# Kernel tuning notes

Hardware: AMD Instinct MI355X
Metric: run time of the kernel (lower is better)

## Reference

```python
import jax, jax.numpy as jnp
import numpy as np


def setup_inputs() -> dict:
    key = jax.random.key(0)
    ks = jax.random.split(key, 10)
    n_cells, n_genes, d, E = 10000, 2000, 128, 2000000
    return {
        "ufeats": jax.random.normal(ks[0], (n_cells, d), jnp.float32),
        "ifeats": jax.random.normal(ks[1], (n_genes, d), jnp.float32),
        "ge_factor": jax.random.uniform(ks[2], (n_genes, 1), jnp.float32),
        "sz_factor": jax.random.uniform(ks[3], (n_cells, 1), jnp.float32),
        "W_mean": jax.random.normal(ks[4], (d, 1), jnp.float32),
        "b_mean": jnp.zeros((1,), jnp.float32),
        "W_disp": jax.random.normal(ks[5], (d, 1), jnp.float32),
        "b_disp": jnp.zeros((1,), jnp.float32),
        "W_pi": jax.random.normal(ks[6], (d, 1), jnp.float32),
        "b_pi": jnp.zeros((1,), jnp.float32),
        "src_idx": jax.random.randint(ks[7], (E,), 0, n_cells, jnp.int64 if jax.config.read('jax_enable_x64') else jnp.int32),
        "dst_idx": jax.random.randint(ks[8], (E,), 0, n_genes, jnp.int64 if jax.config.read('jax_enable_x64') else jnp.int32),
    }


def reference(ufeats, ifeats, ge_factor, sz_factor,
              W_mean, b_mean, W_disp, b_disp, W_pi, b_pi,
              src_idx, dst_idx):
    # u_mul_v('h','h'): per-edge elementwise product of cell (u) and gene (v) feats -> [E, d]
    h_d = ufeats[src_idx] * ifeats[dst_idx]
    mu_ = jax.nn.sigmoid(h_d @ W_mean + b_mean)   # dec_mean: Linear + Sigmoid -> [E, 1]
    disp_ = h_d @ W_disp + b_disp                  # dec_disp: Linear -> [E, 1]
    pi = jax.nn.sigmoid(h_d @ W_pi + b_pi)         # dec_pi: Linear + Sigmoid -> [E, 1]
    gef = ge_factor[dst_idx]                       # u_mul_v('one','ge_factor') -> gene factor per edge
    szf = sz_factor[src_idx]                       # u_mul_v('sz_factor','one') -> cell size factor per edge
    disp = jnp.clip(jax.nn.softplus(gef * disp_), 1e-4, 1e4)          # DispAct
    mu = szf * jnp.clip(jnp.exp(gef * mu_) - 1.0, 1e-5, 1e6)          # MeanAct * sz_factor
    return (mu, disp, pi)
```

## Files before the change

kernel.cpp:

```cpp
#include <hip/hip_runtime.h>
#include <math.h>


typedef _Float16 f16x8 __attribute__((ext_vector_type(8)));
typedef float f32x4 __attribute__((ext_vector_type(4)));
typedef _Float16 h2 __attribute__((ext_vector_type(2)));
union U16 { uint4 u; f16x8 v; };
union HU { uint u; h2 h; };

__global__ __launch_bounds__(256) void cvt_f16_fused_kernel(
    const float4* __restrict__ srcA, int nA4,
    const float4* __restrict__ srcB, int nB4,
    uint2* __restrict__ dst)
{
    int i = blockIdx.x * blockDim.x + threadIdx.x;
    if (i >= nA4 + nB4) return;
    float4 f = (i < nA4) ? srcA[i] : srcB[i - nA4];
    HU a, b;
    a.h = h2{(_Float16)f.x, (_Float16)f.y};
    b.h = h2{(_Float16)f.z, (_Float16)f.w};
    dst[i] = make_uint2(a.u, b.u);
}

__global__ __launch_bounds__(256, 4) void zinb_mfma_lds_kernel(
    const _Float16* __restrict__ uhalf,
    const _Float16* __restrict__ ihalf,
    const float* __restrict__ ge_factor,
    const float* __restrict__ sz_factor,
    const float* __restrict__ W_mean, const float* __restrict__ b_mean,
    const float* __restrict__ W_disp, const float* __restrict__ b_disp,
    const float* __restrict__ W_pi,   const float* __restrict__ b_pi,
    const int* __restrict__ src_idx,
    const int* __restrict__ dst_idx,
    float* __restrict__ out,
    int E)
{
    const int tid  = threadIdx.x;
    const int lane = tid & 63;
    const int col  = lane & 15;
    const int kg   = lane >> 4;
    const int w    = (blockIdx.x * blockDim.x + tid) >> 6;
    const int nw   = (gridDim.x * blockDim.x) >> 6;
    const int ntiles = E >> 4;

    __shared__ __align__(16) _Float16 hsm[4][2048];
    char* const lds = (char*)hsm[tid >> 6];

    const char* const ubase = (const char*)uhalf;
    const char* const vbase = (const char*)ihalf;

    f16x8 bfrag[4];
    {
        const float* Wsel = (col == 0) ? W_mean : (col == 1) ? W_disp : W_pi;
#pragma unroll
        for (int c = 0; c < 4; ++c) {
            f16x8 b;
#pragma unroll
            for (int i = 0; i < 8; ++i) {
                const float wv = Wsel[32 * c + 8 * kg + i];
                b[i] = (col < 3) ? (_Float16)wv : (_Float16)0.f;
            }
            bfrag[c] = b;
        }
    }
    const float bm = b_mean[0], bd = b_disp[0], bp = b_pi[0];

    int wofs[4], rofs[4];
#pragma unroll
    for (int j = 0; j < 4; ++j) {
        const int row = kg + 4 * j;
        wofs[j] = row * 256 + ((col * 16) ^ ((row & 7) << 4));
    }
#pragma unroll
    for (int c = 0; c < 4; ++c)
        rofs[c] = col * 256 + (((c << 6) + (kg << 4)) ^ ((col & 7) << 4));

    int se_c = 0, de_c = 0, se_n = 0, de_n = 0;
    U16 uR[4], vR[4];
    if (w < ntiles) {
        se_c = src_idx[(w << 4) + col];
        de_c = dst_idx[(w << 4) + col];
#pragma unroll
        for (int j = 0; j < 4; ++j) {
            const int ur = __shfl(se_c, kg + 4 * j, 64);
            const int vr = __shfl(de_c, kg + 4 * j, 64);
            uR[j].u = *(const uint4*)(ubase + (unsigned)ur * 256u + (unsigned)col * 16u);
            vR[j].u = *(const uint4*)(vbase + (unsigned)vr * 256u + (unsigned)col * 16u);
        }
        int tn = w + nw; if (tn >= ntiles) tn = w;
        se_n = src_idx[(tn << 4) + col];
        de_n = dst_idx[(tn << 4) + col];
    }

    for (int t = w; t < ntiles; t += nw) {
#pragma unroll
        for (int j = 0; j < 4; ++j) {
            U16 h; h.v = uR[j].v * vR[j].v;
            *(uint4*)(lds + wofs[j]) = h.u;
        }

#pragma unroll
        for (int j = 0; j < 4; ++j) {
            const int ur = __shfl(se_n, kg + 4 * j, 64);
            const int vr = __shfl(de_n, kg + 4 * j, 64);
            uR[j].u = *(const uint4*)(ubase + (unsigned)ur * 256u + (unsigned)col * 16u);
            vR[j].u = *(const uint4*)(vbase + (unsigned)vr * 256u + (unsigned)col * 16u);
        }

        int t2 = t + 2 * nw; if (t2 >= ntiles) t2 = t;
        const int se_n2 = src_idx[(t2 << 4) + col];
        const int de_n2 = dst_idx[(t2 << 4) + col];

        U16 a0, a1, a2, a3;
        a0.u = *(const uint4*)(lds + rofs[0]);
        a1.u = *(const uint4*)(lds + rofs[1]);
        a2.u = *(const uint4*)(lds + rofs[2]);
        a3.u = *(const uint4*)(lds + rofs[3]);

        f32x4 acc = {0.f, 0.f, 0.f, 0.f};
        acc = __builtin_amdgcn_mfma_f32_16x16x32_f16(a0.v, bfrag[0], acc, 0, 0, 0);
        acc = __builtin_amdgcn_mfma_f32_16x16x32_f16(a1.v, bfrag[1], acc, 0, 0, 0);
        acc = __builtin_amdgcn_mfma_f32_16x16x32_f16(a2.v, bfrag[2], acc, 0, 0, 0);
        acc = __builtin_amdgcn_mfma_f32_16x16x32_f16(a3.v, bfrag[3], acc, 0, 0, 0);

        const int e0   = t << 4;
        const int base = kg << 2;
        const int s0 = __shfl(se_c, base + 0, 64);
        const int s1 = __shfl(se_c, base + 1, 64);
        const int s2 = __shfl(se_c, base + 2, 64);
        const int s3 = __shfl(se_c, base + 3, 64);
        const int g0 = __shfl(de_c, base + 0, 64);
        const int g1 = __shfl(de_c, base + 1, 64);
        const int g2 = __shfl(de_c, base + 2, 64);
        const int g3 = __shfl(de_c, base + 3, 64);

        if (col == 0) {
            const float ge0 = ge_factor[g0], ge1 = ge_factor[g1],
                        ge2 = ge_factor[g2], ge3 = ge_factor[g3];
            const float sz0 = sz_factor[s0], sz1 = sz_factor[s1],
                        sz2 = sz_factor[s2], sz3 = sz_factor[s3];
            float4 o;
            o.x = sz0 * fminf(fmaxf(__expf(ge0 / (1.f + __expf(-(acc[0] + bm)))) - 1.f, 1e-5f), 1e6f);
            o.y = sz1 * fminf(fmaxf(__expf(ge1 / (1.f + __expf(-(acc[1] + bm)))) - 1.f, 1e-5f), 1e6f);
            o.z = sz2 * fminf(fmaxf(__expf(ge2 / (1.f + __expf(-(acc[2] + bm)))) - 1.f, 1e-5f), 1e6f);
            o.w = sz3 * fminf(fmaxf(__expf(ge3 / (1.f + __expf(-(acc[3] + bm)))) - 1.f, 1e-5f), 1e6f);
            *(float4*)(out + e0 + base) = o;
        } else if (col == 1) {
            const float ge0 = ge_factor[g0], ge1 = ge_factor[g1],
                        ge2 = ge_factor[g2], ge3 = ge_factor[g3];
            float4 o;
            {
                const float xd = ge0 * (acc[0] + bd);
                o.x = fminf(fmaxf(fmaxf(xd, 0.f) + __logf(1.f + __expf(-fabsf(xd))), 1e-4f), 1e4f);
            }
            {
                const float xd = ge1 * (acc[1] + bd);
                o.y = fminf(fmaxf(fmaxf(xd, 0.f) + __logf(1.f + __expf(-fabsf(xd))), 1e-4f), 1e4f);
            }
            {
                const float xd = ge2 * (acc[2] + bd);
                o.z = fminf(fmaxf(fmaxf(xd, 0.f) + __logf(1.f + __expf(-fabsf(xd))), 1e-4f), 1e4f);
            }
            {
                const float xd = ge3 * (acc[3] + bd);
                o.w = fminf(fmaxf(fmaxf(xd, 0.f) + __logf(1.f + __expf(-fabsf(xd))), 1e-4f), 1e4f);
            }
            *(float4*)(out + (size_t)E + e0 + base) = o;
        } else if (col == 2) {
            float4 o;
            o.x = 1.f / (1.f + __expf(-(acc[0] + bp)));
            o.y = 1.f / (1.f + __expf(-(acc[1] + bp)));
            o.z = 1.f / (1.f + __expf(-(acc[2] + bp)));
            o.w = 1.f / (1.f + __expf(-(acc[3] + bp)));
            *(float4*)(out + (size_t)2 * E + e0 + base) = o;
        }

        se_c = se_n; de_c = de_n; se_n = se_n2; de_n = de_n2;
    }
}

__global__ void zinb_tail_kernel(
    const float* __restrict__ ufeats, const float* __restrict__ ifeats,
    const float* __restrict__ ge_factor, const float* __restrict__ sz_factor,
    const float* __restrict__ W_mean, const float* __restrict__ b_mean,
    const float* __restrict__ W_disp, const float* __restrict__ b_disp,
    const float* __restrict__ W_pi,   const float* __restrict__ b_pi,
    const int* __restrict__ src_idx, const int* __restrict__ dst_idx,
    float* __restrict__ out, int E, int start)
{
    int e = start + blockIdx.x * blockDim.x + threadIdx.x;
    if (e >= E) return;
    const int s = src_idx[e], g = dst_idx[e];
    float am = 0.f, ad = 0.f, ap = 0.f;
    for (int k = 0; k < 128; ++k) {
        float h = ufeats[(size_t)s * 128 + k] * ifeats[(size_t)g * 128 + k];
        am = fmaf(h, W_mean[k], am);
        ad = fmaf(h, W_disp[k], ad);
        ap = fmaf(h, W_pi[k],   ap);
    }
    const float gef = ge_factor[g];
    const float szf = sz_factor[s];
    const float mu_ = 1.f / (1.f + __expf(-(am + b_mean[0])));
    const float pi  = 1.f / (1.f + __expf(-(ap + b_pi[0])));
    const float xd  = gef * (ad + b_disp[0]);
    const float sp  = fmaxf(xd, 0.f) + __logf(1.f + __expf(-fabsf(xd)));
    const float disp = fminf(fmaxf(sp, 1e-4f), 1e4f);
    const float mu = szf * fminf(fmaxf(__expf(gef * mu_) - 1.f, 1e-5f), 1e6f);
    out[e] = mu; out[(size_t)E + e] = disp; out[(size_t)2 * E + e] = pi;
}

__global__ __launch_bounds__(256) void zinb_edge_f32_kernel(
    const float* __restrict__ ufeats, const float* __restrict__ ifeats,
    const float* __restrict__ ge_factor, const float* __restrict__ sz_factor,
    const float* __restrict__ W_mean, const float* __restrict__ b_mean,
    const float* __restrict__ W_disp, const float* __restrict__ b_disp,
    const float* __restrict__ W_pi,   const float* __restrict__ b_pi,
    const int* __restrict__ src_idx, const int* __restrict__ dst_idx,
    float* __restrict__ out, int E)
{
    const int r = threadIdx.x & 7;
    const int slot = (blockIdx.x * blockDim.x + threadIdx.x) >> 3;
    const int n_slots = (gridDim.x * blockDim.x) >> 3;

    float4 wm[4], wd[4], wp[4];
    {
        const float4* wm4 = (const float4*)W_mean + r;
        const float4* wd4 = (const float4*)W_disp + r;
        const float4* wp4 = (const float4*)W_pi   + r;
#pragma unroll
        for (int c = 0; c < 4; ++c) { wm[c] = wm4[c*8]; wd[c] = wd4[c*8]; wp[c] = wp4[c*8]; }
    }
    const float bm = b_mean[0], bd = b_disp[0], bp = b_pi[0];

    for (int e = slot; e < E; e += n_slots) {
        const int s = src_idx[e];
        const int g = dst_idx[e];
        const float4* u4 = (const float4*)(ufeats + (size_t)s * 128) + r;
        const float4* v4 = (const float4*)(ifeats + (size_t)g * 128) + r;
        float am = 0.f, ad = 0.f, ap = 0.f;
#pragma unroll
        for (int c = 0; c < 4; ++c) {
            float4 u = u4[c*8]; float4 v = v4[c*8];
            float px = u.x*v.x, py = u.y*v.y, pz = u.z*v.z, pw = u.w*v.w;
            am = fmaf(px, wm[c].x, am); am = fmaf(py, wm[c].y, am);
            am = fmaf(pz, wm[c].z, am); am = fmaf(pw, wm[c].w, am);
            ad = fmaf(px, wd[c].x, ad); ad = fmaf(py, wd[c].y, ad);
            ad = fmaf(pz, wd[c].z, ad); ad = fmaf(pw, wd[c].w, ad);
            ap = fmaf(px, wp[c].x, ap); ap = fmaf(py, wp[c].y, ap);
            ap = fmaf(pz, wp[c].z, ap); ap = fmaf(pw, wp[c].w, ap);
        }
#pragma unroll
        for (int off = 1; off < 8; off <<= 1) {
            am += __shfl_xor(am, off); ad += __shfl_xor(ad, off); ap += __shfl_xor(ap, off);
        }
        if (r == 0) {
            const float gef = ge_factor[g];
            const float szf = sz_factor[s];
            const float mu_ = 1.f / (1.f + __expf(-(am + bm)));
            const float pi  = 1.f / (1.f + __expf(-(ap + bp)));
            const float xd  = gef * (ad + bd);
            const float sp  = fmaxf(xd, 0.f) + __logf(1.f + __expf(-fabsf(xd)));
            const float disp = fminf(fmaxf(sp, 1e-4f), 1e4f);
            const float mu = szf * fminf(fmaxf(__expf(gef * mu_) - 1.f, 1e-5f), 1e6f);
            out[e] = mu; out[(size_t)E + e] = disp; out[(size_t)2*E + e] = pi;
        }
    }
}

extern "C" void kernel_launch(void* const* d_in, const int* in_sizes, int n_in,
                              void* d_out, int out_size, void* d_ws, size_t ws_size,
                              hipStream_t stream) {
    const float* ufeats    = (const float*)d_in[0];
    const float* ifeats    = (const float*)d_in[1];
    const float* ge_factor = (const float*)d_in[2];
    const float* sz_factor = (const float*)d_in[3];
    const float* W_mean    = (const float*)d_in[4];
    const float* b_mean    = (const float*)d_in[5];
    const float* W_disp    = (const float*)d_in[6];
    const float* b_disp    = (const float*)d_in[7];
    const float* W_pi      = (const float*)d_in[8];
    const float* b_pi      = (const float*)d_in[9];
    const int*   src_idx   = (const int*)d_in[10];
    const int*   dst_idx   = (const int*)d_in[11];
    float* out = (float*)d_out;

    const int E       = in_sizes[10];
    const int n_cells = in_sizes[0] / 128;
    const int n_genes = in_sizes[1] / 128;

    const size_t u_elems = (size_t)n_cells * 128;
    const size_t i_elems = (size_t)n_genes * 128;
    const size_t ws_needed = (u_elems + i_elems) * sizeof(_Float16);

    if (ws_size >= ws_needed && (E & 3) == 0) {
        _Float16* uhalf = (_Float16*)d_ws;
        _Float16* ihalf = uhalf + u_elems;

        const int un4 = (int)(u_elems / 4);
        const int in4 = (int)(i_elems / 4);
        const int n4  = un4 + in4;
        hipLaunchKernelGGL(cvt_f16_fused_kernel, dim3((n4 + 255) / 256), dim3(256), 0, stream,
                           (const float4*)ufeats, un4, (const float4*)ifeats, in4,
                           (uint2*)d_ws);

        hipLaunchKernelGGL(zinb_mfma_lds_kernel, dim3(2048), dim3(256), 0, stream,
                           uhalf, ihalf, ge_factor, sz_factor,
                           W_mean, b_mean, W_disp, b_disp, W_pi, b_pi,
                           src_idx, dst_idx, out, E);

        const int rem = E & 15;
        if (rem) {
            hipLaunchKernelGGL(zinb_tail_kernel, dim3(1), dim3(64), 0, stream,
                               ufeats, ifeats, ge_factor, sz_factor,
                               W_mean, b_mean, W_disp, b_disp, W_pi, b_pi,
                               src_idx, dst_idx, out, E, E - rem);
        }
    } else {
        hipLaunchKernelGGL(zinb_edge_f32_kernel, dim3(2048), dim3(256), 0, stream,
                           ufeats, ifeats, ge_factor, sz_factor,
                           W_mean, b_mean, W_disp, b_disp, W_pi, b_pi,
                           src_idx, dst_idx, out, E);
    }
}
```

Baseline: 168.0 us.

## Process 64 edges per wave iteration with LDS-staged epilogue across all lanes

Each wave now handles a 64-edge super-tile as four 16-edge MFMA sub-tiles. It loads indices once per lane for 64 edges and pipelines the gathers of the next sub-tile behind the current MFMA. MFMA results are written to a small LDS buffer, so the activation epilogue runs on all 64 lanes, one edge per lane, instead of only 3 of 16 columns doing four edges each. This is meant to remove the lane-divergent epilogue and the per-sub-tile shuffle and index overhead. The cost is extra LDS traffic and larger unrolled code with more register pressure.

```diff
diff --git a/kernel.cpp b/kernel.cpp
--- a/kernel.cpp
+++ b/kernel.cpp
@@ -22,7 +22,36 @@
     dst[i] = make_uint2(a.u, b.u);
 }
 
-__global__ __launch_bounds__(256, 4) void zinb_mfma_lds_kernel(
+#define STAGE(S, SEV, DEV) {                                                  \
+    _Pragma("unroll")                                                         \
+    for (int j = 0; j < 4; ++j) {                                             \
+        const int ur = __shfl((SEV), 16 * (S) + 4 * kg + j, 64);              \
+        const int vr = __shfl((DEV), 16 * (S) + 4 * kg + j, 64);              \
+        uR[j].u = *(const uint4*)(ubase + (unsigned)ur * 256u + col16);       \
+        vR[j].u = *(const uint4*)(vbase + (unsigned)vr * 256u + col16);       \
+    } }
+
+#define TILE(S, STAGE_STMT) {                                                 \
+    U16 hh0, hh1, hh2, hh3;                                                   \
+    hh0.v = uR[0].v * vR[0].v; hh1.v = uR[1].v * vR[1].v;                     \
+    hh2.v = uR[2].v * vR[2].v; hh3.v = uR[3].v * vR[3].v;                     \
+    *(uint4*)(lds + wofs[0]) = hh0.u; *(uint4*)(lds + wofs[1]) = hh1.u;       \
+    *(uint4*)(lds + wofs[2]) = hh2.u; *(uint4*)(lds + wofs[3]) = hh3.u;       \
+    STAGE_STMT;                                                               \
+    U16 a0, a1, a2, a3;                                                       \
+    a0.u = *(const uint4*)(lds + rofs[0]);                                    \
+    a1.u = *(const uint4*)(lds + rofs[1]);                                    \
+    a2.u = *(const uint4*)(lds + rofs[2]);                                    \
+    a3.u = *(const uint4*)(lds + rofs[3]);                                    \
+    f32x4 acc = {0.f, 0.f, 0.f, 0.f};                                         \
+    acc = __builtin_amdgcn_mfma_f32_16x16x32_f16(a0.v, bfrag[0], acc, 0, 0, 0);\
+    acc = __builtin_amdgcn_mfma_f32_16x16x32_f16(a1.v, bfrag[1], acc, 0, 0, 0);\
+    acc = __builtin_amdgcn_mfma_f32_16x16x32_f16(a2.v, bfrag[2], acc, 0, 0, 0);\
+    acc = __builtin_amdgcn_mfma_f32_16x16x32_f16(a3.v, bfrag[3], acc, 0, 0, 0);\
+    if (col < 3) *(f32x4*)((char*)ols + col * 256 + (S) * 64 + kg * 16) = acc;\
+    }
+
+__global__ __launch_bounds__(256, 4) void zinb_mfma64_kernel(
     const _Float16* __restrict__ uhalf,
     const _Float16* __restrict__ ihalf,
     const float* __restrict__ ge_factor,
@@ -39,12 +68,15 @@
     const int lane = tid & 63;
     const int col  = lane & 15;
     const int kg   = lane >> 4;
+    const unsigned col16 = (unsigned)col * 16u;
     const int w    = (blockIdx.x * blockDim.x + tid) >> 6;
     const int nw   = (gridDim.x * blockDim.x) >> 6;
-    const int ntiles = E >> 4;
+    const int NT   = E >> 6;
 
     __shared__ __align__(16) _Float16 hsm[4][2048];
-    char* const lds = (char*)hsm[tid >> 6];
+    __shared__ __align__(16) float    osm[4][192];
+    char*  const lds = (char*)hsm[tid >> 6];
+    float* const ols = osm[tid >> 6];
 
     const char* const ubase = (const char*)uhalf;
     const char* const vbase = (const char*)ihalf;
@@ -68,7 +100,7 @@
     int wofs[4], rofs[4];
 #pragma unroll
     for (int j = 0; j < 4; ++j) {
-        const int row = kg + 4 * j;
+        const int row = 4 * kg + j;
         wofs[j] = row * 256 + ((col * 16) ^ ((row & 7) << 4));
     }
 #pragma unroll
@@ -77,103 +109,43 @@
 
     int se_c = 0, de_c = 0, se_n = 0, de_n = 0;
     U16 uR[4], vR[4];
-    if (w < ntiles) {
-        se_c = src_idx[(w << 4) + col];
-        de_c = dst_idx[(w << 4) + col];
-#pragma unroll
-        for (int j = 0; j < 4; ++j) {
-            const int ur = __shfl(se_c, kg + 4 * j, 64);
-            const int vr = __shfl(de_c, kg + 4 * j, 64);
-            uR[j].u = *(const uint4*)(ubase + (unsigned)ur * 256u + (unsigned)col * 16u);
-            vR[j].u = *(const uint4*)(vbase + (unsigned)vr * 256u + (unsigned)col * 16u);
-        }
-        int tn = w + nw; if (tn >= ntiles) tn = w;
-        se_n = src_idx[(tn << 4) + col];
-        de_n = dst_idx[(tn << 4) + col];
-    }
-
-    for (int t = w; t < ntiles; t += nw) {
-#pragma unroll
-        for (int j = 0; j < 4; ++j) {
-            U16 h; h.v = uR[j].v * vR[j].v;
-            *(uint4*)(lds + wofs[j]) = h.u;
-        }
-
-#pragma unroll
-        for (int j = 0; j < 4; ++j) {
-            const int ur = __shfl(se_n, kg + 4 * j, 64);
-            const int vr = __shfl(de_n, kg + 4 * j, 64);
-            uR[j].u = *(const uint4*)(ubase + (unsigned)ur * 256u + (unsigned)col * 16u);
-            vR[j].u = *(const uint4*)(vbase + (unsigned)vr * 256u + (unsigned)col * 16u);
-        }
-
-        int t2 = t + 2 * nw; if (t2 >= ntiles) t2 = t;
-        const int se_n2 = src_idx[(t2 << 4) + col];
-        const int de_n2 = dst_idx[(t2 << 4) + col];
-
-        U16 a0, a1, a2, a3;
-        a0.u = *(const uint4*)(lds + rofs[0]);
-        a1.u = *(const uint4*)(lds + rofs[1]);
-        a2.u = *(const uint4*)(lds + rofs[2]);
-        a3.u = *(const uint4*)(lds + rofs[3]);
-
-        f32x4 acc = {0.f, 0.f, 0.f, 0.f};
-        acc = __builtin_amdgcn_mfma_f32_16x16x32_f16(a0.v, bfrag[0], acc, 0, 0, 0);
-        acc = __builtin_amdgcn_mfma_f32_16x16x32_f16(a1.v, bfrag[1], acc, 0, 0, 0);
-        acc = __builtin_amdgcn_mfma_f32_16x16x32_f16(a2.v, bfrag[2], acc, 0, 0, 0);
-        acc = __builtin_amdgcn_mfma_f32_16x16x32_f16(a3.v, bfrag[3], acc, 0, 0, 0);
-
-        const int e0   = t << 4;
-        const int base = kg << 2;
-        const int s0 = __shfl(se_c, base + 0, 64);
-        const int s1 = __shfl(se_c, base + 1, 64);
-        const int s2 = __shfl(se_c, base + 2, 64);
-        const int s3 = __shfl(se_c, base + 3, 64);
-        const int g0 = __shfl(de_c, base + 0, 64);
-        const int g1 = __shfl(de_c, base + 1, 64);
-        const int g2 = __shfl(de_c, base + 2, 64);
-        const int g3 = __shfl(de_c, base + 3, 64);
-
-        if (col == 0) {
-            const float ge0 = ge_factor[g0], ge1 = ge_factor[g1],
-                        ge2 = ge_factor[g2], ge3 = ge_factor[g3];
-            const float sz0 = sz_factor[s0], sz1 = sz_factor[s1],
-                        sz2 = sz_factor[s2], sz3 = sz_factor[s3];
-            float4 o;
-            o.x = sz0 * fminf(fmaxf(__expf(ge0 / (1.f + __expf(-(acc[0] + bm)))) - 1.f, 1e-5f), 1e6f);
-            o.y = sz1 * fminf(fmaxf(__expf(ge1 / (1.f + __expf(-(acc[1] + bm)))) - 1.f, 1e-5f), 1e6f);
-            o.z = sz2 * fminf(fmaxf(__expf(ge2 / (1.f + __expf(-(acc[2] + bm)))) - 1.f, 1e-5f), 1e6f);
-            o.w = sz3 * fminf(fmaxf(__expf(ge3 / (1.f + __expf(-(acc[3] + bm)))) - 1.f, 1e-5f), 1e6f);
-            *(float4*)(out + e0 + base) = o;
-        } else if (col == 1) {
-            const float ge0 = ge_factor[g0], ge1 = ge_factor[g1],
-                        ge2 = ge_factor[g2], ge3 = ge_factor[g3];
-            float4 o;
-            {
-                const float xd = ge0 * (acc[0] + bd);
-                o.x = fminf(fmaxf(fmaxf(xd, 0.f) + __logf(1.f + __expf(-fabsf(xd))), 1e-4f), 1e4f);
-            }
-            {
-                const float xd = ge1 * (acc[1] + bd);
-                o.y = fminf(fmaxf(fmaxf(xd, 0.f) + __logf(1.f + __expf(-fabsf(xd))), 1e-4f), 1e4f);
-            }
-            {
-                const float xd = ge2 * (acc[2] + bd);
-                o.z = fminf(fmaxf(fmaxf(xd, 0.f) + __logf(1.f + __expf(-fabsf(xd))), 1e-4f), 1e4f);
-            }
-            {
-                const float xd = ge3 * (acc[3] + bd);
-                o.w = fminf(fmaxf(fmaxf(xd, 0.f) + __logf(1.f + __expf(-fabsf(xd))), 1e-4f), 1e4f);
-            }
-            *(float4*)(out + (size_t)E + e0 + base) = o;
-        } else if (col == 2) {
-            float4 o;
-            o.x = 1.f / (1.f + __expf(-(acc[0] + bp)));
-            o.y = 1.f / (1.f + __expf(-(acc[1] + bp)));
-            o.z = 1.f / (1.f + __expf(-(acc[2] + bp)));
-            o.w = 1.f / (1.f + __expf(-(acc[3] + bp)));
-            *(float4*)(out + (size_t)2 * E + e0 + base) = o;
-        }
+    if (w < NT) {
+        se_c = src_idx[(w << 6) + lane];
+        de_c = dst_idx[(w << 6) + lane];
+        int tn = w + nw; if (tn >= NT) tn = w;
+        se_n = src_idx[(tn << 6) + lane];
+        de_n = dst_idx[(tn << 6) + lane];
+        STAGE(0, se_c, de_c)
+    }
+
+    for (int t = w; t < NT; t += nw) {
+        int t2 = t + 2 * nw; if (t2 >= NT) t2 = t;
+        const int se_n2 = src_idx[(t2 << 6) + lane];
+        const int de_n2 = dst_idx[(t2 << 6) + lane];
+
+        TILE(0, STAGE(1, se_c, de_c))
+        TILE(1, STAGE(2, se_c, de_c))
+        TILE(2, STAGE(3, se_c, de_c))
+        TILE(3, STAGE(0, se_n, de_n))
+
+        const int e0 = t << 6;
+        const float m  = ols[lane];
+        const float dd = ols[64 + lane];
+        const float pp = ols[128 + lane];
+        const float gef = ge_factor[de_c];
+        const float szf = sz_factor[se_c];
+
+        const float mu_ = 1.f / (1.f + __expf(-(m + bm)));
+        const float pi  = 1.f / (1.f + __expf(-(pp + bp)));
+        const float xd  = gef * (dd + bd);
+        const float sp  = fmaxf(xd, 0.f) + __logf(1.f + __expf(-fabsf(xd)));
+        const float disp = fminf(fmaxf(sp, 1e-4f), 1e4f);
+        const float mu = szf * fminf(fmaxf(__expf(gef * mu_) - 1.f, 1e-5f), 1e6f);
+
+        const int e = e0 + lane;
+        out[e]                 = mu;
+        out[(size_t)E + e]     = disp;
+        out[(size_t)2 * E + e] = pi;
 
         se_c = se_n; de_c = de_n; se_n = se_n2; de_n = de_n2;
     }
@@ -247,7 +219,7 @@
             ad = fmaf(px, wd[c].x, ad); ad = fmaf(py, wd[c].y, ad);
             ad = fmaf(pz, wd[c].z, ad); ad = fmaf(pw, wd[c].w, ad);
             ap = fmaf(px, wp[c].x, ap); ap = fmaf(py, wp[c].y, ap);
-            ap = fmaf(pz, wp[c].z, ap); ap = fmaf(pw, wp[c].w, ap);
+            ap = fmaf(pw, wp[c].w, ap); ap = fmaf(pz, wp[c].z, ap);
         }
 #pragma unroll
         for (int off = 1; off < 8; off <<= 1) {
@@ -292,7 +264,7 @@
     const size_t i_elems = (size_t)n_genes * 128;
     const size_t ws_needed = (u_elems + i_elems) * sizeof(_Float16);
 
-    if (ws_size >= ws_needed && (E & 3) == 0) {
+    if (ws_size >= ws_needed) {
         _Float16* uhalf = (_Float16*)d_ws;
         _Float16* ihalf = uhalf + u_elems;
 
@@ -303,12 +275,12 @@
                            (const float4*)ufeats, un4, (const float4*)ifeats, in4,
                            (uint2*)d_ws);
 
-        hipLaunchKernelGGL(zinb_mfma_lds_kernel, dim3(2048), dim3(256), 0, stream,
+        hipLaunchKernelGGL(zinb_mfma64_kernel, dim3(2048), dim3(256), 0, stream,
                            uhalf, ihalf, ge_factor, sz_factor,
                            W_mean, b_mean, W_disp, b_disp, W_pi, b_pi,
                            src_idx, dst_idx, out, E);
 
-        const int rem = E & 15;
+        const int rem = E & 63;
         if (rem) {
             hipLaunchKernelGGL(zinb_tail_kernel, dim3(1), dim3(64), 0, stream,
                                ufeats, ifeats, ge_factor, sz_factor,
```

New measurement: 143.1 us. 1.17x faster.
